# Kernel tuning notes

Hardware: AMD Instinct MI355X
Metric: run time of the kernel (lower is better)

## Reference

```python
import jax, jax.numpy as jnp
import numpy as np

N, H, C, G = 50000, 16, 8, 128   # nodes, heads, per-head channels, graphs
F_IN, NUM_CLASSES = 128, 2
E = 800000
HC = H * C
NEG_SLOPE = 0.2
BN_EPS = 1e-5


def setup_inputs() -> dict:
    key = jax.random.key(0)
    ks = jax.random.split(key, 32)
    s = 0.1
    p = lambda k, shape: (jax.random.normal(k, shape, jnp.float32) * s)
    inp = {
        "x": jax.random.normal(ks[0], (N, F_IN), jnp.float32),
        "edge_index": jax.random.randint(ks[1], (2, E), 0, N, dtype=jnp.int32),
        "batch": jnp.sort(jax.random.randint(ks[2], (N,), 0, G, dtype=jnp.int32)),
        # GAT layer 1 (in=F_IN)
        "W1": p(ks[3], (F_IN, HC)), "b1": p(ks[4], (HC,)),
        "asrc1": p(ks[5], (H, C)), "adst1": p(ks[6], (H, C)),
        "g1": 1.0 + p(ks[7], (HC,)), "beta1": p(ks[8], (HC,)),
        # GAT layer 2 (in=HC)
        "W2": p(ks[9], (HC, HC)), "b2": p(ks[10], (HC,)),
        "asrc2": p(ks[11], (H, C)), "adst2": p(ks[12], (H, C)),
        "g2": 1.0 + p(ks[13], (HC,)), "beta2": p(ks[14], (HC,)),
        # GAT layer 3
        "W3": p(ks[15], (HC, HC)), "b3": p(ks[16], (HC,)),
        "asrc3": p(ks[17], (H, C)), "adst3": p(ks[18], (H, C)),
        "g3": 1.0 + p(ks[19], (HC,)), "beta3": p(ks[20], (HC,)),
        # final linear + bn4
        "Wl": p(ks[21], (2 * HC, NUM_CLASSES)), "bl": p(ks[22], (NUM_CLASSES,)),
        "g4": 1.0 + p(ks[23], (NUM_CLASSES,)), "beta4": p(ks[24], (NUM_CLASSES,)),
    }
    return inp


def _gat(x, src, dst, W, b, asrc, adst):
    # x: [N, F_in] -> h: [N, H, C]
    h = (x @ W).reshape(N, H, C)
    a_s = jnp.einsum("nhc,hc->nh", h, asrc)  # [N,H]
    a_d = jnp.einsum("nhc,hc->nh", h, adst)
    e = jax.nn.leaky_relu(a_s[src] + a_d[dst], NEG_SLOPE)  # [E',H]
    # per-destination softmax (every node has a self loop -> segments non-empty)
    e_max = jax.ops.segment_max(e, dst, num_segments=N)
    ex = jnp.exp(e - e_max[dst])
    denom = jax.ops.segment_sum(ex, dst, num_segments=N)
    alpha = ex / (denom[dst] + 1e-16)  # [E',H]
    out = jax.ops.segment_sum(h[src] * alpha[:, :, None], dst, num_segments=N)
    return out.reshape(N, HC) + b


def _bn(x, g, beta):
    mu = jnp.mean(x, axis=0)
    var = jnp.mean((x - mu) ** 2, axis=0)  # biased, training-mode BN
    return (x - mu) * jax.lax.rsqrt(var + BN_EPS) * g + beta


def reference(x, edge_index, batch,
              W1, b1, asrc1, adst1, g1, beta1,
              W2, b2, asrc2, adst2, g2, beta2,
              W3, b3, asrc3, adst3, g3, beta3,
              Wl, bl, g4, beta4):
    # add self loops once (add_self_loops=True in every GATConv)
    loop = jnp.arange(N, dtype=edge_index.dtype)
    src = jnp.concatenate([edge_index[0], loop])
    dst = jnp.concatenate([edge_index[1], loop])

    h = jax.nn.relu(_bn(_gat(x, src, dst, W1, b1, asrc1, adst1), g1, beta1))
    h = jax.nn.relu(_bn(_gat(h, src, dst, W2, b2, asrc2, adst2), g2, beta2))
    h = jax.nn.relu(_bn(_gat(h, src, dst, W3, b3, asrc3, adst3), g3, beta3))

    pooled_sum = jax.ops.segment_sum(h, batch, num_segments=G)        # [G,HC]
    cnt = jax.ops.segment_sum(jnp.ones((N,), h.dtype), batch, num_segments=G)
    pooled_mean = pooled_sum / jnp.maximum(cnt, 1.0)[:, None]
    z = jnp.concatenate([pooled_mean, pooled_sum], axis=1)            # [G,2*HC]
    z = z @ Wl + bl
    return _bn(z, g4, beta4)
```

## Files before the change

kernel.cpp:

```cpp
#include <hip/hip_runtime.h>

#define NN 50000
#define NHEADS 16
#define NGRAPH 128
#define NEDGE 800000
#define NEP (NEDGE + NN)

#define EPB 2048
#define NBLK 416
#define NBUK 391
#define CASTB 3125
#define WTB 192
#define WASB 48

typedef float4 f4;
typedef __attribute__((ext_vector_type(4))) float f32x4;
typedef __attribute__((ext_vector_type(8))) short s8;

__device__ inline unsigned short f2b(float f) {
  union { float f; unsigned u; } v; v.f = f;
  unsigned r = v.u + 0x7FFFu + ((v.u >> 16) & 1u);
  return (unsigned short)(r >> 16);
}
__device__ inline float b2f(unsigned u16) {
  union { unsigned u; float f; } v; v.u = u16 << 16;
  return v.f;
}
__device__ inline float blo(unsigned u) {
  union { unsigned u; float f; } v; v.u = u << 16;
  return v.f;
}
__device__ inline float bhi(unsigned u) {
  union { unsigned u; float f; } v; v.u = u & 0xffff0000u;
  return v.f;
}


__global__ __launch_bounds__(256) void k_bhist(const int* __restrict__ ei, int* __restrict__ cntmat) {
  __shared__ int hist[NBUK];
  int t = threadIdx.x, b = blockIdx.x;
  for (int k = t; k < NBUK; k += 256) hist[k] = 0;
  __syncthreads();
  int i0 = b * EPB;
  int i1 = i0 + EPB < NEP ? i0 + EPB : NEP;
  for (int i = i0 + t; i < i1; i += 256) {
    int d = (i < NEDGE) ? ei[NEDGE + i] : (i - NEDGE);
    atomicAdd(&hist[d >> 7], 1);
  }
  __syncthreads();
  for (int k = t; k < NBUK; k += 256) cntmat[b * NBUK + k] = hist[k];
}

__global__ __launch_bounds__(512) void k_bscan(int* __restrict__ cntmat, int* __restrict__ btotal) {
  __shared__ int buf[512];
  int t = threadIdx.x, k = blockIdx.x;
  int v = (t < NBLK) ? cntmat[t * NBUK + k] : 0;
  buf[t] = v;
  __syncthreads();
  for (int off = 1; off < 512; off <<= 1) {
    int y = (t >= off) ? buf[t - off] : 0;
    __syncthreads();
    buf[t] += y;
    __syncthreads();
  }
  if (t < NBLK) cntmat[t * NBUK + k] = buf[t] - v;
  if (t == 511) btotal[k] = buf[511];
}

__global__ __launch_bounds__(512) void k_bbase(const int* __restrict__ btotal, int* __restrict__ bbase) {
  __shared__ int buf[512];
  int t = threadIdx.x;
  int v = (t < NBUK) ? btotal[t] : 0;
  buf[t] = v;
  __syncthreads();
  for (int off = 1; off < 512; off <<= 1) {
    int y = (t >= off) ? buf[t - off] : 0;
    __syncthreads();
    buf[t] += y;
    __syncthreads();
  }
  if (t < NBUK) bbase[t] = buf[t] - v;
  if (t == 511) bbase[NBUK] = buf[511];
}

__global__ __launch_bounds__(256) void k_bscatter(const int* __restrict__ ei, const int* __restrict__ cntmat,
                                                  const int* __restrict__ bbase, unsigned* __restrict__ pairs) {
  __shared__ int cur[NBUK];
  int t = threadIdx.x, b = blockIdx.x;
  for (int k = t; k < NBUK; k += 256) cur[k] = bbase[k] + cntmat[b * NBUK + k];
  __syncthreads();
  int i0 = b * EPB;
  int i1 = i0 + EPB < NEP ? i0 + EPB : NEP;
  for (int i = i0 + t; i < i1; i += 256) {
    int s, d;
    if (i < NEDGE) { s = ei[i]; d = ei[NEDGE + i]; }
    else { s = d = i - NEDGE; }
    int pos = atomicAdd(&cur[d >> 7], 1);
    pairs[pos] = ((unsigned)(d & 127) << 16) | (unsigned)s;
  }
}

__global__ __launch_bounds__(256) void k_bfinal(const unsigned* __restrict__ pairs, const int* __restrict__ bbase,
                                                int* __restrict__ row_off, int* __restrict__ colp) {
  __shared__ int cnt[128];
  __shared__ int buf[128];
  __shared__ int cur[128];
  int t = threadIdx.x, k = blockIdx.x;
  int n0 = k << 7;
  if (t < 128) cnt[t] = 0;
  __syncthreads();
  int p0 = bbase[k], p1 = bbase[k + 1];
  for (int i = p0 + t; i < p1; i += 256) atomicAdd(&cnt[pairs[i] >> 16], 1);
  __syncthreads();
  if (t < 128) buf[t] = cnt[t];
  __syncthreads();
  for (int off = 1; off < 128; off <<= 1) {
    int y = (t < 128 && t >= off) ? buf[t - off] : 0;
    __syncthreads();
    if (t < 128) buf[t] += y;
    __syncthreads();
  }
  if (t < 128) {
    int excl = buf[t] - cnt[t];
    cur[t] = p0 + excl;
    if (n0 + t < NN) row_off[n0 + t] = p0 + excl;
  }
  if (k == NBUK - 1 && t == 0) row_off[NN] = p1;
  __syncthreads();
  for (int i = p0 + t; i < p1; i += 256) {
    unsigned r = pairs[i];
    int pos = atomicAdd(&cur[r >> 16], 1);
    colp[pos] = (int)(r & 0xffffu);
  }
}


__global__ __launch_bounds__(256) void k_prep(const float* __restrict__ X, unsigned short* __restrict__ Xb,
                                              const float* __restrict__ W0, const float* __restrict__ W1, const float* __restrict__ W2,
                                              const float* __restrict__ as0, const float* __restrict__ as1, const float* __restrict__ as2,
                                              const float* __restrict__ ad0, const float* __restrict__ ad1, const float* __restrict__ ad2,
                                              unsigned short* __restrict__ T0, unsigned short* __restrict__ T1, unsigned short* __restrict__ T2,
                                              const int* __restrict__ batch, int* __restrict__ gstart) {
  int b = blockIdx.x, t = threadIdx.x;
  if (b < CASTB) {
    int i = b * 256 + t;
    const f4* X4 = (const f4*)X;
    f4 a = X4[2 * i], c = X4[2 * i + 1];
    uint4 o;
    o.x = (unsigned)f2b(a.x) | ((unsigned)f2b(a.y) << 16);
    o.y = (unsigned)f2b(a.z) | ((unsigned)f2b(a.w) << 16);
    o.z = (unsigned)f2b(c.x) | ((unsigned)f2b(c.y) << 16);
    o.w = (unsigned)f2b(c.z) | ((unsigned)f2b(c.w) << 16);
    ((uint4*)Xb)[i] = o;
  } else if (b < CASTB + WTB) {
    int idx = (b - CASTB) * 256 + t;
    int L = idx >> 14, r = idx & 16383;
    int n = r >> 7, kk = r & 127;
    const float* W = (L == 0) ? W0 : (L == 1) ? W1 : W2;
    unsigned short* T = (L == 0) ? T0 : (L == 1) ? T1 : T2;
    T[n * 128 + kk] = f2b(W[kk * 128 + n]);
  } else if (b < CASTB + WTB + WASB) {
    int idx = (b - CASTB - WTB) * 256 + t;
    int L = idx >> 12, r = idx & 4095;
    int h2 = r >> 7, kk = r & 127;
    int h = h2 & 15;
    const float* W = (L == 0) ? W0 : (L == 1) ? W1 : W2;
    const float* av = (h2 < 16) ? ((L == 0) ? as0 : (L == 1) ? as1 : as2)
                                : ((L == 0) ? ad0 : (L == 1) ? ad1 : ad2);
    unsigned short* T = (L == 0) ? T0 : (L == 1) ? T1 : T2;
    float s = 0.f;
#pragma unroll
    for (int c = 0; c < 8; ++c) s += W[kk * 128 + h * 8 + c] * av[h * 8 + c];
    T[(128 + h2) * 128 + kk] = f2b(s);
  } else {
    int g = t;
    if (g > NGRAPH) return;
    int lo = 0, hi = NN;
    while (lo < hi) { int mid = (lo + hi) >> 1; if (batch[mid] < g) lo = mid + 1; else hi = mid; }
    gstart[g] = lo;
  }
}


template<int FUSE>
__global__ __launch_bounds__(256) void k_gemm_t(const unsigned short* __restrict__ A, const unsigned short* __restrict__ Wt,
                                                const float* __restrict__ sc, unsigned short* __restrict__ Hb,
                                                unsigned short* __restrict__ Asb, float* __restrict__ Ad) {
  int w = threadIdx.x >> 6, l = threadIdx.x & 63;
  int r0 = blockIdx.x * 128 + w * 32;
  int lr = l & 15, lg = l >> 4;
  f32x4 acc[2][10];
#pragma unroll
  for (int m = 0; m < 2; ++m)
#pragma unroll
    for (int n = 0; n < 10; ++n) acc[m][n] = (f32x4){0.f, 0.f, 0.f, 0.f};

#pragma unroll
  for (int ks = 0; ks < 4; ++ks) {
    int koff = ks * 32 + lg * 8;
    s8 a[2];
    if constexpr (FUSE) {
      f4 s0 = *(const f4*)(sc + koff),       s1 = *(const f4*)(sc + koff + 4);
      f4 h0 = *(const f4*)(sc + 128 + koff), h1 = *(const f4*)(sc + 128 + koff + 4);
#pragma unroll
      for (int m = 0; m < 2; ++m) {
        int row = r0 + m * 16 + lr;
        row = (row < NN) ? row : (NN - 1);
        uint4 raw = *(const uint4*)(A + (size_t)row * 128 + koff);
        float v0 = fmaxf(blo(raw.x) * s0.x + h0.x, 0.f);
        float v1 = fmaxf(bhi(raw.x) * s0.y + h0.y, 0.f);
        float v2 = fmaxf(blo(raw.y) * s0.z + h0.z, 0.f);
        float v3 = fmaxf(bhi(raw.y) * s0.w + h0.w, 0.f);
        float v4 = fmaxf(blo(raw.z) * s1.x + h1.x, 0.f);
        float v5 = fmaxf(bhi(raw.z) * s1.y + h1.y, 0.f);
        float v6 = fmaxf(blo(raw.w) * s1.z + h1.z, 0.f);
        float v7 = fmaxf(bhi(raw.w) * s1.w + h1.w, 0.f);
        union { s8 v; uint4 u; } pk;
        pk.u.x = (unsigned)f2b(v0) | ((unsigned)f2b(v1) << 16);
        pk.u.y = (unsigned)f2b(v2) | ((unsigned)f2b(v3) << 16);
        pk.u.z = (unsigned)f2b(v4) | ((unsigned)f2b(v5) << 16);
        pk.u.w = (unsigned)f2b(v6) | ((unsigned)f2b(v7) << 16);
        a[m] = pk.v;
      }
    } else {
#pragma unroll
      for (int m = 0; m < 2; ++m) {
        int row = r0 + m * 16 + lr;
        row = (row < NN) ? row : (NN - 1);
        a[m] = *(const s8*)(A + (size_t)row * 128 + koff);
      }
    }
#pragma unroll
    for (int n = 0; n < 10; ++n) {
      s8 b = *(const s8*)(Wt + (size_t)(n * 16 + lr) * 128 + koff);
#pragma unroll
      for (int m = 0; m < 2; ++m)
        acc[m][n] = __builtin_amdgcn_mfma_f32_16x16x32_bf16(a[m], b, acc[m][n], 0, 0, 0);
    }
  }

#pragma unroll
  for (int m = 0; m < 2; ++m) {
    int rowb = r0 + m * 16 + lg * 4;
#pragma unroll
    for (int n = 0; n < 8; ++n) {
      int colb = n * 16 + lr;
#pragma unroll
      for (int reg = 0; reg < 4; ++reg) {
        int row = rowb + reg;
        if (row < NN) Hb[(size_t)row * 128 + colb] = f2b(acc[m][n][reg]);
      }
    }
#pragma unroll
    for (int reg = 0; reg < 4; ++reg) {
      int row = rowb + reg;
      if (row < NN) {
        Asb[row * 16 + lr] = f2b(acc[m][8][reg]);
        Ad[row * 16 + lr] = acc[m][9][reg];
      }
    }
  }
}


__global__ __launch_bounds__(256, 4) void k_agg(const unsigned short* __restrict__ Hb, const unsigned short* __restrict__ Asb,
                                                const float* __restrict__ Ad,
                                                const int* __restrict__ row_off, const int* __restrict__ col,
                                                unsigned short* __restrict__ Vb) {
  int node = blockIdx.x * 16 + (threadIdx.x >> 4);
  int h = threadIdx.x & 15;
  int e0 = row_off[node], e1 = row_off[node + 1];
  float adh = Ad[node * 16 + h];
  float den = 0.f;
  float acc[8] = {0.f, 0.f, 0.f, 0.f, 0.f, 0.f, 0.f, 0.f};
  int j = e0;
  for (; j + 7 < e1; j += 8) {
    int s[8];
#pragma unroll
    for (int q = 0; q < 8; ++q) s[q] = col[j + q];
    float a[8];
#pragma unroll
    for (int q = 0; q < 8; ++q) a[q] = b2f(Asb[s[q] * 16 + h]);
    uint4 p[8];
#pragma unroll
    for (int q = 0; q < 8; ++q) p[q] = *(const uint4*)(Hb + (size_t)s[q] * 128 + h * 8);
#pragma unroll
    for (int q = 0; q < 8; ++q) {
      float e = a[q] + adh;
      e = (e > 0.f) ? e : 0.2f * e;
      a[q] = __expf(e);
      den += a[q];
    }
#pragma unroll
    for (int q = 0; q < 8; ++q) {
      acc[0] += a[q] * blo(p[q].x); acc[1] += a[q] * bhi(p[q].x);
      acc[2] += a[q] * blo(p[q].y); acc[3] += a[q] * bhi(p[q].y);
      acc[4] += a[q] * blo(p[q].z); acc[5] += a[q] * bhi(p[q].z);
      acc[6] += a[q] * blo(p[q].w); acc[7] += a[q] * bhi(p[q].w);
    }
  }
  for (; j + 3 < e1; j += 4) {
    int s[4];
#pragma unroll
    for (int q = 0; q < 4; ++q) s[q] = col[j + q];
    float a[4];
#pragma unroll
    for (int q = 0; q < 4; ++q) a[q] = b2f(Asb[s[q] * 16 + h]);
    uint4 p[4];
#pragma unroll
    for (int q = 0; q < 4; ++q) p[q] = *(const uint4*)(Hb + (size_t)s[q] * 128 + h * 8);
#pragma unroll
    for (int q = 0; q < 4; ++q) {
      float e = a[q] + adh;
      e = (e > 0.f) ? e : 0.2f * e;
      a[q] = __expf(e);
      den += a[q];
    }
#pragma unroll
    for (int q = 0; q < 4; ++q) {
      acc[0] += a[q] * blo(p[q].x); acc[1] += a[q] * bhi(p[q].x);
      acc[2] += a[q] * blo(p[q].y); acc[3] += a[q] * bhi(p[q].y);
      acc[4] += a[q] * blo(p[q].z); acc[5] += a[q] * bhi(p[q].z);
      acc[6] += a[q] * blo(p[q].w); acc[7] += a[q] * bhi(p[q].w);
    }
  }
  for (; j < e1; ++j) {
    int s0 = col[j];
    float a0 = b2f(Asb[s0 * 16 + h]) + adh;
    uint4 p0 = *(const uint4*)(Hb + (size_t)s0 * 128 + h * 8);
    a0 = (a0 > 0.f) ? a0 : 0.2f * a0;
    float x0 = __expf(a0);
    den += x0;
    acc[0] += x0 * blo(p0.x); acc[1] += x0 * bhi(p0.x);
    acc[2] += x0 * blo(p0.y); acc[3] += x0 * bhi(p0.y);
    acc[4] += x0 * blo(p0.z); acc[5] += x0 * bhi(p0.z);
    acc[6] += x0 * blo(p0.w); acc[7] += x0 * bhi(p0.w);
  }
  float inv = 1.f / (den + 1e-16f);
  uint4 o;
  o.x = (unsigned)f2b(acc[0] * inv) | ((unsigned)f2b(acc[1] * inv) << 16);
  o.y = (unsigned)f2b(acc[2] * inv) | ((unsigned)f2b(acc[3] * inv) << 16);
  o.z = (unsigned)f2b(acc[4] * inv) | ((unsigned)f2b(acc[5] * inv) << 16);
  o.w = (unsigned)f2b(acc[6] * inv) | ((unsigned)f2b(acc[7] * inv) << 16);
  *(uint4*)(Vb + (size_t)node * 128 + h * 8) = o;
}


#define BN_CHUNK 391

__global__ __launch_bounds__(256) void k_bnreduce(const unsigned short* __restrict__ Vb, float* __restrict__ partS, float* __restrict__ partQ) {
  int t = threadIdx.x;
  int c4 = t & 31, rs = t >> 5;
  int r0 = blockIdx.x * BN_CHUNK + rs;
  int rend = blockIdx.x * BN_CHUNK + BN_CHUNK;
  if (rend > NN) rend = NN;
  float s0 = 0.f, s1 = 0.f, s2 = 0.f, s3 = 0.f;
  float q0 = 0.f, q1 = 0.f, q2 = 0.f, q3 = 0.f;
  for (int r = r0; r < rend; r += 8) {
    uint2 p = *(const uint2*)(Vb + (size_t)r * 128 + c4 * 4);
    float v0 = blo(p.x), v1 = bhi(p.x);
    float v2 = blo(p.y), v3 = bhi(p.y);
    s0 += v0; s1 += v1; s2 += v2; s3 += v3;
    q0 += v0 * v0; q1 += v1 * v1; q2 += v2 * v2; q3 += v3 * v3;
  }
  __shared__ float sm[8][32][8];
  sm[rs][c4][0] = s0; sm[rs][c4][1] = s1; sm[rs][c4][2] = s2; sm[rs][c4][3] = s3;
  sm[rs][c4][4] = q0; sm[rs][c4][5] = q1; sm[rs][c4][6] = q2; sm[rs][c4][7] = q3;
  __syncthreads();
  if (t < 32) {
#pragma unroll
    for (int k = 0; k < 4; ++k) {
      float S = 0.f, Q = 0.f;
#pragma unroll
      for (int r = 0; r < 8; ++r) { S += sm[r][t][k]; Q += sm[r][t][4 + k]; }
      partS[blockIdx.x * 128 + t * 4 + k] = S;
      partQ[blockIdx.x * 128 + t * 4 + k] = Q;
    }
  }
}

__global__ __launch_bounds__(512) void k_bnfin(const float* __restrict__ partS, const float* __restrict__ partQ,
                                               const float* __restrict__ gam, const float* __restrict__ bet,
                                               float* __restrict__ sc) {
  int t = threadIdx.x;
  int c = t & 127, q = (t >> 7) & 1, hf = t >> 8;
  const float* src = q ? partQ : partS;
  float s = 0.f;
#pragma unroll 8
  for (int i = hf * 64; i < hf * 64 + 64; ++i) s += src[i * 128 + c];
  __shared__ float sm[512];
  sm[t] = s;
  __syncthreads();
  if (t < 128) {
    float S = sm[t] + sm[t + 256];
    float Q = sm[t + 128] + sm[t + 384];
    float mean = S * (1.f / NN);
    float var = fmaxf(Q * (1.f / NN) - mean * mean, 0.f);
    float sg = gam[t] * rsqrtf(var + 1e-5f);
    sc[t] = sg;
    sc[128 + t] = bet[t] - mean * sg;
  }
}


__global__ __launch_bounds__(256) void k_pool(const unsigned short* __restrict__ Vb, const float* __restrict__ sc,
                                              const int* __restrict__ gstart, float* __restrict__ pp) {
  int g = blockIdx.x >> 2, chunk = blockIdx.x & 3;
  int t = threadIdx.x;
  int c4 = t & 31, rs = t >> 5;
  f4 s = ((const f4*)sc)[c4], sh = ((const f4*)sc)[32 + c4];
  int r0 = gstart[g], r1 = gstart[g + 1];
  float s0 = 0.f, s1 = 0.f, s2 = 0.f, s3 = 0.f;
  for (int r = r0 + chunk + 4 * rs; r < r1; r += 32) {
    uint2 p = *(const uint2*)(Vb + (size_t)r * 128 + c4 * 4);
    s0 += fmaxf(blo(p.x) * s.x + sh.x, 0.f);
    s1 += fmaxf(bhi(p.x) * s.y + sh.y, 0.f);
    s2 += fmaxf(blo(p.y) * s.z + sh.z, 0.f);
    s3 += fmaxf(bhi(p.y) * s.w + sh.w, 0.f);
  }
  __shared__ float sm[8][32][4];
  sm[rs][c4][0] = s0; sm[rs][c4][1] = s1; sm[rs][c4][2] = s2; sm[rs][c4][3] = s3;
  __syncthreads();
  if (t < 32) {
#pragma unroll
    for (int k = 0; k < 4; ++k) {
      float S = 0.f;
#pragma unroll
      for (int r = 0; r < 8; ++r) S += sm[r][t][k];
      pp[(size_t)blockIdx.x * 128 + t * 4 + k] = S;
    }
  }
}

__global__ __launch_bounds__(256) void k_final(const float* __restrict__ pp, const int* __restrict__ gstart,
                                               const float* __restrict__ Wl, const float* __restrict__ bl,
                                               const float* __restrict__ g4, const float* __restrict__ b4,
                                               float* __restrict__ out) {
  int t = threadIdx.x;
  int g = t >> 1, cls = t & 1;
  float cnt = fmaxf((float)(gstart[g + 1] - gstart[g]), 1.f);
  float inv = 1.f / cnt;
  float z = bl[cls];
  for (int f = 0; f < 128; ++f) {
    float ps = pp[(size_t)(g * 4 + 0) * 128 + f] + pp[(size_t)(g * 4 + 1) * 128 + f]
             + pp[(size_t)(g * 4 + 2) * 128 + f] + pp[(size_t)(g * 4 + 3) * 128 + f];
    z += ps * inv * Wl[f * 2 + cls] + ps * Wl[(128 + f) * 2 + cls];
  }
  __shared__ float zs[256];
  __shared__ float st[4];
  zs[t] = z;
  __syncthreads();
  if (t < 2) {
    float s = 0.f, s2 = 0.f;
    for (int gg = 0; gg < 128; ++gg) { float v = zs[gg * 2 + t]; s += v; s2 += v * v; }
    float mean = s * (1.f / 128.f);
    float var = s2 * (1.f / 128.f) - mean * mean;
    var = fmaxf(var, 0.f);
    float sc = g4[t] * rsqrtf(var + 1e-5f);
    st[t] = sc; st[2 + t] = b4[t] - mean * sc;
  }
  __syncthreads();
  out[t] = zs[t] * st[cls] + st[2 + cls];
}


extern "C" void kernel_launch(void* const* d_in, const int* in_sizes, int n_in,
                              void* d_out, int out_size, void* d_ws, size_t ws_size,
                              hipStream_t stream) {
  const float* x     = (const float*)d_in[0];
  const int*   ei    = (const int*)d_in[1];
  const int*   batch = (const int*)d_in[2];
  const float* W[3]    = {(const float*)d_in[3],  (const float*)d_in[9],  (const float*)d_in[15]};
  const float* asrc[3] = {(const float*)d_in[5],  (const float*)d_in[11], (const float*)d_in[17]};
  const float* adst[3] = {(const float*)d_in[6],  (const float*)d_in[12], (const float*)d_in[18]};
  const float* gam[3]  = {(const float*)d_in[7],  (const float*)d_in[13], (const float*)d_in[19]};
  const float* bet[3]  = {(const float*)d_in[8],  (const float*)d_in[14], (const float*)d_in[20]};
  const float* Wl    = (const float*)d_in[21];
  const float* bl    = (const float*)d_in[22];
  const float* g4    = (const float*)d_in[23];
  const float* beta4 = (const float*)d_in[24];

  char* ws = (char*)d_ws;
  size_t off = 0;
  auto alloc = [&](size_t bytes) -> void* {
    void* p = (void*)(ws + off);
    off += (bytes + 255) & ~(size_t)255;
    return p;
  };

  int* row_off  = (int*)alloc((size_t)(NN + 1) * 4);
  int* col      = (int*)alloc((size_t)NEP * 4);
  int* cntmat   = (int*)alloc((size_t)NBLK * NBUK * 4);
  int* btotal   = (int*)alloc((size_t)NBUK * 4);
  int* bbase    = (int*)alloc((size_t)(NBUK + 1) * 4);
  unsigned* pairs = (unsigned*)alloc((size_t)NEP * 4);
  unsigned short* Xb = (unsigned short*)alloc((size_t)NN * 128 * 2);
  unsigned short* Hb = (unsigned short*)alloc((size_t)NN * 128 * 2);
  unsigned short* Vb = (unsigned short*)alloc((size_t)NN * 128 * 2);
  unsigned short* Asb = (unsigned short*)alloc((size_t)NN * 16 * 2);
  float* Ad     = (float*)alloc((size_t)NN * 16 * 4);
  unsigned short* Wt0 = (unsigned short*)alloc((size_t)160 * 128 * 2);
  unsigned short* Wt1 = (unsigned short*)alloc((size_t)160 * 128 * 2);
  unsigned short* Wt2 = (unsigned short*)alloc((size_t)160 * 128 * 2);
  const unsigned short* Wt[3] = {Wt0, Wt1, Wt2};
  float* partS  = (float*)alloc(128 * 128 * 4);
  float* partQ  = (float*)alloc(128 * 128 * 4);
  float* bn_sc  = (float*)alloc(256 * 4);
  float* pp     = (float*)alloc((size_t)NGRAPH * 4 * 128 * 4);
  int* gstart   = (int*)alloc((size_t)(NGRAPH + 1) * 4);

  k_bhist<<<NBLK, 256, 0, stream>>>(ei, cntmat);
  k_bscan<<<NBUK, 512, 0, stream>>>(cntmat, btotal);
  k_bbase<<<1, 512, 0, stream>>>(btotal, bbase);
  k_bscatter<<<NBLK, 256, 0, stream>>>(ei, cntmat, bbase, pairs);
  k_bfinal<<<NBUK, 256, 0, stream>>>(pairs, bbase, row_off, col);

  k_prep<<<CASTB + WTB + WASB + 1, 256, 0, stream>>>(x, Xb, W[0], W[1], W[2],
                                                     asrc[0], asrc[1], asrc[2], adst[0], adst[1], adst[2],
                                                     Wt0, Wt1, Wt2, batch, gstart);

  for (int L = 0; L < 3; ++L) {
    if (L == 0)
      k_gemm_t<0><<<(NN + 127) / 128, 256, 0, stream>>>(Xb, Wt[L], nullptr, Hb, Asb, Ad);
    else
      k_gemm_t<1><<<(NN + 127) / 128, 256, 0, stream>>>(Vb, Wt[L], bn_sc, Hb, Asb, Ad);
    k_agg<<<NN / 16, 256, 0, stream>>>(Hb, Asb, Ad, row_off, col, Vb);
    k_bnreduce<<<128, 256, 0, stream>>>(Vb, partS, partQ);
    k_bnfin<<<1, 512, 0, stream>>>(partS, partQ, gam[L], bet[L], bn_sc);
  }

  k_pool<<<NGRAPH * 4, 256, 0, stream>>>(Vb, bn_sc, gstart, pp);
  k_final<<<1, 256, 0, stream>>>(pp, gstart, Wl, bl, g4, beta4, (float*)d_out);
}
```

Measured before the change: 297.4 us.

## Split GAT aggregation edges across two half-warps with double-buffered loads

The aggregation kernel now gives each destination node 32 lanes: two groups of 16 heads each take alternating edges, and their partial sums and denominators are combined with a lane shuffle. The main loop is software-pipelined with two register buffers, so the gathers for the next 4 edges are issued before the current 4 are consumed. The aim is more memory-level parallelism and less serial latency per node, since average degree is about 17. The costs are twice as many threads and blocks, extra shuffles, half the lanes idle during the store, and higher register pressure from the double buffers.

New measurement: 301.9 us. About the same (+1.5%).

```diff
diff --git a/kernel.cpp b/kernel.cpp
--- a/kernel.cpp
+++ b/kernel.cpp
@@ -263,68 +263,57 @@
 }
 
 
+#define AGG_LOAD(S, A, P) do { \
+  _Pragma("unroll") for (int q = 0; q < 4; ++q) S[q] = col[j + 2 * q]; \
+  _Pragma("unroll") for (int q = 0; q < 4; ++q) A[q] = b2f(Asb[S[q] * 16 + h]); \
+  _Pragma("unroll") for (int q = 0; q < 4; ++q) P[q] = *(const uint4*)(Hb + (size_t)S[q] * 128 + h * 8); \
+  j += 8; } while (0)
+
+#define AGG_CONSUME(A, P) do { \
+  _Pragma("unroll") for (int q = 0; q < 4; ++q) { \
+    float e = A[q] + adh; e = (e > 0.f) ? e : 0.2f * e; A[q] = __expf(e); den += A[q]; } \
+  _Pragma("unroll") for (int q = 0; q < 4; ++q) { \
+    acc[0] += A[q] * blo(P[q].x); acc[1] += A[q] * bhi(P[q].x); \
+    acc[2] += A[q] * blo(P[q].y); acc[3] += A[q] * bhi(P[q].y); \
+    acc[4] += A[q] * blo(P[q].z); acc[5] += A[q] * bhi(P[q].z); \
+    acc[6] += A[q] * blo(P[q].w); acc[7] += A[q] * bhi(P[q].w); } } while (0)
+
 __global__ __launch_bounds__(256, 4) void k_agg(const unsigned short* __restrict__ Hb, const unsigned short* __restrict__ Asb,
                                                 const float* __restrict__ Ad,
                                                 const int* __restrict__ row_off, const int* __restrict__ col,
                                                 unsigned short* __restrict__ Vb) {
-  int node = blockIdx.x * 16 + (threadIdx.x >> 4);
-  int h = threadIdx.x & 15;
+  int node = blockIdx.x * 8 + (threadIdx.x >> 5);
+  int l = threadIdx.x & 31;
+  int h = l & 15, par = l >> 4;
   int e0 = row_off[node], e1 = row_off[node + 1];
   float adh = Ad[node * 16 + h];
   float den = 0.f;
   float acc[8] = {0.f, 0.f, 0.f, 0.f, 0.f, 0.f, 0.f, 0.f};
-  int j = e0;
-  for (; j + 7 < e1; j += 8) {
-    int s[8];
-#pragma unroll
-    for (int q = 0; q < 8; ++q) s[q] = col[j + q];
-    float a[8];
-#pragma unroll
-    for (int q = 0; q < 8; ++q) a[q] = b2f(Asb[s[q] * 16 + h]);
-    uint4 p[8];
-#pragma unroll
-    for (int q = 0; q < 8; ++q) p[q] = *(const uint4*)(Hb + (size_t)s[q] * 128 + h * 8);
-#pragma unroll
-    for (int q = 0; q < 8; ++q) {
-      float e = a[q] + adh;
-      e = (e > 0.f) ? e : 0.2f * e;
-      a[q] = __expf(e);
-      den += a[q];
-    }
-#pragma unroll
-    for (int q = 0; q < 8; ++q) {
-      acc[0] += a[q] * blo(p[q].x); acc[1] += a[q] * bhi(p[q].x);
-      acc[2] += a[q] * blo(p[q].y); acc[3] += a[q] * bhi(p[q].y);
-      acc[4] += a[q] * blo(p[q].z); acc[5] += a[q] * bhi(p[q].z);
-      acc[6] += a[q] * blo(p[q].w); acc[7] += a[q] * bhi(p[q].w);
-    }
-  }
-  for (; j + 3 < e1; j += 4) {
-    int s[4];
-#pragma unroll
-    for (int q = 0; q < 4; ++q) s[q] = col[j + q];
-    float a[4];
-#pragma unroll
-    for (int q = 0; q < 4; ++q) a[q] = b2f(Asb[s[q] * 16 + h]);
-    uint4 p[4];
-#pragma unroll
-    for (int q = 0; q < 4; ++q) p[q] = *(const uint4*)(Hb + (size_t)s[q] * 128 + h * 8);
-#pragma unroll
-    for (int q = 0; q < 4; ++q) {
-      float e = a[q] + adh;
-      e = (e > 0.f) ? e : 0.2f * e;
-      a[q] = __expf(e);
-      den += a[q];
-    }
-#pragma unroll
-    for (int q = 0; q < 4; ++q) {
-      acc[0] += a[q] * blo(p[q].x); acc[1] += a[q] * bhi(p[q].x);
-      acc[2] += a[q] * blo(p[q].y); acc[3] += a[q] * bhi(p[q].y);
-      acc[4] += a[q] * blo(p[q].z); acc[5] += a[q] * bhi(p[q].z);
-      acc[6] += a[q] * blo(p[q].w); acc[7] += a[q] * bhi(p[q].w);
-    }
-  }
-  for (; j < e1; ++j) {
+  int j = e0 + par;
+
+  int sA[4]; float aA[4]; uint4 pA[4];
+  int sB[4]; float aB[4]; uint4 pB[4];
+  (void)sA; (void)sB;
+  if (j + 6 < e1) {
+    AGG_LOAD(sA, aA, pA);
+    for (;;) {
+      if (j + 6 < e1) {
+        AGG_LOAD(sB, aB, pB);
+        AGG_CONSUME(aA, pA);
+      } else {
+        AGG_CONSUME(aA, pA);
+        break;
+      }
+      if (j + 6 < e1) {
+        AGG_LOAD(sA, aA, pA);
+        AGG_CONSUME(aB, pB);
+      } else {
+        AGG_CONSUME(aB, pB);
+        break;
+      }
+    }
+  }
+  for (; j < e1; j += 2) {
     int s0 = col[j];
     float a0 = b2f(Asb[s0 * 16 + h]) + adh;
     uint4 p0 = *(const uint4*)(Hb + (size_t)s0 * 128 + h * 8);
@@ -336,13 +325,18 @@
     acc[4] += x0 * blo(p0.z); acc[5] += x0 * bhi(p0.z);
     acc[6] += x0 * blo(p0.w); acc[7] += x0 * bhi(p0.w);
   }
-  float inv = 1.f / (den + 1e-16f);
-  uint4 o;
-  o.x = (unsigned)f2b(acc[0] * inv) | ((unsigned)f2b(acc[1] * inv) << 16);
-  o.y = (unsigned)f2b(acc[2] * inv) | ((unsigned)f2b(acc[3] * inv) << 16);
-  o.z = (unsigned)f2b(acc[4] * inv) | ((unsigned)f2b(acc[5] * inv) << 16);
-  o.w = (unsigned)f2b(acc[6] * inv) | ((unsigned)f2b(acc[7] * inv) << 16);
-  *(uint4*)(Vb + (size_t)node * 128 + h * 8) = o;
+  den += __shfl_xor(den, 16);
+#pragma unroll
+  for (int k = 0; k < 8; ++k) acc[k] += __shfl_xor(acc[k], 16);
+  if (par == 0) {
+    float inv = 1.f / (den + 1e-16f);
+    uint4 o;
+    o.x = (unsigned)f2b(acc[0] * inv) | ((unsigned)f2b(acc[1] * inv) << 16);
+    o.y = (unsigned)f2b(acc[2] * inv) | ((unsigned)f2b(acc[3] * inv) << 16);
+    o.z = (unsigned)f2b(acc[4] * inv) | ((unsigned)f2b(acc[5] * inv) << 16);
+    o.w = (unsigned)f2b(acc[6] * inv) | ((unsigned)f2b(acc[7] * inv) << 16);
+    *(uint4*)(Vb + (size_t)node * 128 + h * 8) = o;
+  }
 }
 
 
@@ -524,7 +518,7 @@
       k_gemm_t<0><<<(NN + 127) / 128, 256, 0, stream>>>(Xb, Wt[L], nullptr, Hb, Asb, Ad);
     else
       k_gemm_t<1><<<(NN + 127) / 128, 256, 0, stream>>>(Vb, Wt[L], bn_sc, Hb, Asb, Ad);
-    k_agg<<<NN / 16, 256, 0, stream>>>(Hb, Asb, Ad, row_off, col, Vb);
+    k_agg<<<NN / 8, 256, 0, stream>>>(Hb, Asb, Ad, row_off, col, Vb);
     k_bnreduce<<<128, 256, 0, stream>>>(Vb, partS, partQ);
     k_bnfin<<<1, 512, 0, stream>>>(partS, partQ, gam[L], bet[L], bn_sc);
   }
```

## Split GAT aggregation by head halves and edge parity; merge histogram with prep kernel

Applied to the files above, without the earlier changes.

The edge-histogram kernel and the input/weight prep kernel are merged into one launch, removing a launch and letting independent work share the GPU. The aggregation kernel now covers each node with two blocks, one per half of the heads. Within a block, two lanes per head take alternating edges, and their partial sums are combined with a cross-lane shuffle. This doubles the number of threads in flight to hide gather latency on high-degree nodes, at the cost of redundant row_off/Ad loads, a shuffle reduction, and a block-index mapping chosen so paired blocks stay adjacent for cache locality.

After: 282.2 us (median of 2 runs). 1.05x faster.

```diff
diff --git a/kernel.cpp b/kernel.cpp
--- a/kernel.cpp
+++ b/kernel.cpp
@@ -36,20 +36,68 @@
 }
 
 
-__global__ __launch_bounds__(256) void k_bhist(const int* __restrict__ ei, int* __restrict__ cntmat) {
+__global__ __launch_bounds__(256) void k_front(const int* __restrict__ ei, int* __restrict__ cntmat,
+                                               const float* __restrict__ X, unsigned short* __restrict__ Xb,
+                                               const float* __restrict__ W0, const float* __restrict__ W1, const float* __restrict__ W2,
+                                               const float* __restrict__ as0, const float* __restrict__ as1, const float* __restrict__ as2,
+                                               const float* __restrict__ ad0, const float* __restrict__ ad1, const float* __restrict__ ad2,
+                                               unsigned short* __restrict__ T0, unsigned short* __restrict__ T1, unsigned short* __restrict__ T2,
+                                               const int* __restrict__ batch, int* __restrict__ gstart) {
   __shared__ int hist[NBUK];
-  int t = threadIdx.x, b = blockIdx.x;
-  for (int k = t; k < NBUK; k += 256) hist[k] = 0;
-  __syncthreads();
-  int i0 = b * EPB;
-  int i1 = i0 + EPB < NEP ? i0 + EPB : NEP;
-  for (int i = i0 + t; i < i1; i += 256) {
-    int d = (i < NEDGE) ? ei[NEDGE + i] : (i - NEDGE);
-    atomicAdd(&hist[d >> 7], 1);
-  }
-  __syncthreads();
-  for (int k = t; k < NBUK; k += 256) cntmat[b * NBUK + k] = hist[k];
-}
+  int b = blockIdx.x, t = threadIdx.x;
+  if (b < NBLK) {
+    for (int k = t; k < NBUK; k += 256) hist[k] = 0;
+    __syncthreads();
+    int i0 = b * EPB;
+    int i1 = i0 + EPB < NEP ? i0 + EPB : NEP;
+    for (int i = i0 + t; i < i1; i += 256) {
+      int d = (i < NEDGE) ? ei[NEDGE + i] : (i - NEDGE);
+      atomicAdd(&hist[d >> 7], 1);
+    }
+    __syncthreads();
+    for (int k = t; k < NBUK; k += 256) cntmat[b * NBUK + k] = hist[k];
+    return;
+  }
+  int pb = b - NBLK;
+  if (pb < CASTB) {
+    int i = pb * 256 + t;
+    const f4* X4 = (const f4*)X;
+    f4 a = X4[2 * i], c = X4[2 * i + 1];
+    uint4 o;
+    o.x = (unsigned)f2b(a.x) | ((unsigned)f2b(a.y) << 16);
+    o.y = (unsigned)f2b(a.z) | ((unsigned)f2b(a.w) << 16);
+    o.z = (unsigned)f2b(c.x) | ((unsigned)f2b(c.y) << 16);
+    o.w = (unsigned)f2b(c.z) | ((unsigned)f2b(c.w) << 16);
+    ((uint4*)Xb)[i] = o;
+  } else if (pb < CASTB + WTB) {
+    int idx = (pb - CASTB) * 256 + t;
+    int L = idx >> 14, r = idx & 16383;
+    int n = r >> 7, kk = r & 127;
+    const float* W = (L == 0) ? W0 : (L == 1) ? W1 : W2;
+    unsigned short* T = (L == 0) ? T0 : (L == 1) ? T1 : T2;
+    T[n * 128 + kk] = f2b(W[kk * 128 + n]);
+  } else if (pb < CASTB + WTB + WASB) {
+    int idx = (pb - CASTB - WTB) * 256 + t;
+    int L = idx >> 12, r = idx & 4095;
+    int h2 = r >> 7, kk = r & 127;
+    int h = h2 & 15;
+    const float* W = (L == 0) ? W0 : (L == 1) ? W1 : W2;
+    const float* av = (h2 < 16) ? ((L == 0) ? as0 : (L == 1) ? as1 : as2)
+                                : ((L == 0) ? ad0 : (L == 1) ? ad1 : ad2);
+    unsigned short* T = (L == 0) ? T0 : (L == 1) ? T1 : T2;
+    float s = 0.f;
+#pragma unroll
+    for (int c = 0; c < 8; ++c) s += W[kk * 128 + h * 8 + c] * av[h * 8 + c];
+    T[(128 + h2) * 128 + kk] = f2b(s);
+  } else {
+    int g = t;
+    if (g > NGRAPH) return;
+    int lo = 0, hi = NN;
+    while (lo < hi) { int mid = (lo + hi) >> 1; if (batch[mid] < g) lo = mid + 1; else hi = mid; }
+    gstart[g] = lo;
+  }
+}
+
 
 __global__ __launch_bounds__(512) void k_bscan(int* __restrict__ cntmat, int* __restrict__ btotal) {
   __shared__ int buf[512];
@@ -131,53 +179,6 @@
     unsigned r = pairs[i];
     int pos = atomicAdd(&cur[r >> 16], 1);
     colp[pos] = (int)(r & 0xffffu);
-  }
-}
-
-
-__global__ __launch_bounds__(256) void k_prep(const float* __restrict__ X, unsigned short* __restrict__ Xb,
-                                              const float* __restrict__ W0, const float* __restrict__ W1, const float* __restrict__ W2,
-                                              const float* __restrict__ as0, const float* __restrict__ as1, const float* __restrict__ as2,
-                                              const float* __restrict__ ad0, const float* __restrict__ ad1, const float* __restrict__ ad2,
-                                              unsigned short* __restrict__ T0, unsigned short* __restrict__ T1, unsigned short* __restrict__ T2,
-                                              const int* __restrict__ batch, int* __restrict__ gstart) {
-  int b = blockIdx.x, t = threadIdx.x;
-  if (b < CASTB) {
-    int i = b * 256 + t;
-    const f4* X4 = (const f4*)X;
-    f4 a = X4[2 * i], c = X4[2 * i + 1];
-    uint4 o;
-    o.x = (unsigned)f2b(a.x) | ((unsigned)f2b(a.y) << 16);
-    o.y = (unsigned)f2b(a.z) | ((unsigned)f2b(a.w) << 16);
-    o.z = (unsigned)f2b(c.x) | ((unsigned)f2b(c.y) << 16);
-    o.w = (unsigned)f2b(c.z) | ((unsigned)f2b(c.w) << 16);
-    ((uint4*)Xb)[i] = o;
-  } else if (b < CASTB + WTB) {
-    int idx = (b - CASTB) * 256 + t;
-    int L = idx >> 14, r = idx & 16383;
-    int n = r >> 7, kk = r & 127;
-    const float* W = (L == 0) ? W0 : (L == 1) ? W1 : W2;
-    unsigned short* T = (L == 0) ? T0 : (L == 1) ? T1 : T2;
-    T[n * 128 + kk] = f2b(W[kk * 128 + n]);
-  } else if (b < CASTB + WTB + WASB) {
-    int idx = (b - CASTB - WTB) * 256 + t;
-    int L = idx >> 12, r = idx & 4095;
-    int h2 = r >> 7, kk = r & 127;
-    int h = h2 & 15;
-    const float* W = (L == 0) ? W0 : (L == 1) ? W1 : W2;
-    const float* av = (h2 < 16) ? ((L == 0) ? as0 : (L == 1) ? as1 : as2)
-                                : ((L == 0) ? ad0 : (L == 1) ? ad1 : ad2);
-    unsigned short* T = (L == 0) ? T0 : (L == 1) ? T1 : T2;
-    float s = 0.f;
-#pragma unroll
-    for (int c = 0; c < 8; ++c) s += W[kk * 128 + h * 8 + c] * av[h * 8 + c];
-    T[(128 + h2) * 128 + kk] = f2b(s);
-  } else {
-    int g = t;
-    if (g > NGRAPH) return;
-    int lo = 0, hi = NN;
-    while (lo < hi) { int mid = (lo + hi) >> 1; if (batch[mid] < g) lo = mid + 1; else hi = mid; }
-    gstart[g] = lo;
   }
 }
 
@@ -267,17 +268,24 @@
                                                 const float* __restrict__ Ad,
                                                 const int* __restrict__ row_off, const int* __restrict__ col,
                                                 unsigned short* __restrict__ Vb) {
-  int node = blockIdx.x * 16 + (threadIdx.x >> 4);
-  int h = threadIdx.x & 15;
+  int b = blockIdx.x;
+  int half = (b >> 2) & 1;
+  int nb = (b >> 3) * 4 + (b & 3);
+  if (nb >= 3125) return;
+  int t = threadIdx.x;
+  int node = nb * 16 + (t >> 4);
+  int l = t & 15;
+  int h = half * 8 + (l & 7);
+  int par = l >> 3;
   int e0 = row_off[node], e1 = row_off[node + 1];
   float adh = Ad[node * 16 + h];
   float den = 0.f;
   float acc[8] = {0.f, 0.f, 0.f, 0.f, 0.f, 0.f, 0.f, 0.f};
-  int j = e0;
-  for (; j + 7 < e1; j += 8) {
+  int j = e0 + par;
+  for (; j + 14 < e1; j += 16) {
     int s[8];
 #pragma unroll
-    for (int q = 0; q < 8; ++q) s[q] = col[j + q];
+    for (int q = 0; q < 8; ++q) s[q] = col[j + 2 * q];
     float a[8];
 #pragma unroll
     for (int q = 0; q < 8; ++q) a[q] = b2f(Asb[s[q] * 16 + h]);
@@ -299,10 +307,10 @@
       acc[6] += a[q] * blo(p[q].w); acc[7] += a[q] * bhi(p[q].w);
     }
   }
-  for (; j + 3 < e1; j += 4) {
+  for (; j + 6 < e1; j += 8) {
     int s[4];
 #pragma unroll
-    for (int q = 0; q < 4; ++q) s[q] = col[j + q];
+    for (int q = 0; q < 4; ++q) s[q] = col[j + 2 * q];
     float a[4];
 #pragma unroll
     for (int q = 0; q < 4; ++q) a[q] = b2f(Asb[s[q] * 16 + h]);
@@ -324,7 +332,7 @@
       acc[6] += a[q] * blo(p[q].w); acc[7] += a[q] * bhi(p[q].w);
     }
   }
-  for (; j < e1; ++j) {
+  for (; j < e1; j += 2) {
     int s0 = col[j];
     float a0 = b2f(Asb[s0 * 16 + h]) + adh;
     uint4 p0 = *(const uint4*)(Hb + (size_t)s0 * 128 + h * 8);
@@ -336,13 +344,18 @@
     acc[4] += x0 * blo(p0.z); acc[5] += x0 * bhi(p0.z);
     acc[6] += x0 * blo(p0.w); acc[7] += x0 * bhi(p0.w);
   }
-  float inv = 1.f / (den + 1e-16f);
-  uint4 o;
-  o.x = (unsigned)f2b(acc[0] * inv) | ((unsigned)f2b(acc[1] * inv) << 16);
-  o.y = (unsigned)f2b(acc[2] * inv) | ((unsigned)f2b(acc[3] * inv) << 16);
-  o.z = (unsigned)f2b(acc[4] * inv) | ((unsigned)f2b(acc[5] * inv) << 16);
-  o.w = (unsigned)f2b(acc[6] * inv) | ((unsigned)f2b(acc[7] * inv) << 16);
-  *(uint4*)(Vb + (size_t)node * 128 + h * 8) = o;
+  den += __shfl_xor(den, 8);
+#pragma unroll
+  for (int k = 0; k < 8; ++k) acc[k] += __shfl_xor(acc[k], 8);
+  if (par == 0) {
+    float inv = 1.f / (den + 1e-16f);
+    uint4 o;
+    o.x = (unsigned)f2b(acc[0] * inv) | ((unsigned)f2b(acc[1] * inv) << 16);
+    o.y = (unsigned)f2b(acc[2] * inv) | ((unsigned)f2b(acc[3] * inv) << 16);
+    o.z = (unsigned)f2b(acc[4] * inv) | ((unsigned)f2b(acc[5] * inv) << 16);
+    o.w = (unsigned)f2b(acc[6] * inv) | ((unsigned)f2b(acc[7] * inv) << 16);
+    *(uint4*)(Vb + (size_t)node * 128 + h * 8) = o;
+  }
 }
 
 
@@ -509,22 +522,20 @@
   float* pp     = (float*)alloc((size_t)NGRAPH * 4 * 128 * 4);
   int* gstart   = (int*)alloc((size_t)(NGRAPH + 1) * 4);
 
-  k_bhist<<<NBLK, 256, 0, stream>>>(ei, cntmat);
+  k_front<<<NBLK + CASTB + WTB + WASB + 1, 256, 0, stream>>>(ei, cntmat, x, Xb, W[0], W[1], W[2],
+                                                             asrc[0], asrc[1], asrc[2], adst[0], adst[1], adst[2],
+                                                             Wt0, Wt1, Wt2, batch, gstart);
   k_bscan<<<NBUK, 512, 0, stream>>>(cntmat, btotal);
   k_bbase<<<1, 512, 0, stream>>>(btotal, bbase);
   k_bscatter<<<NBLK, 256, 0, stream>>>(ei, cntmat, bbase, pairs);
   k_bfinal<<<NBUK, 256, 0, stream>>>(pairs, bbase, row_off, col);
-
-  k_prep<<<CASTB + WTB + WASB + 1, 256, 0, stream>>>(x, Xb, W[0], W[1], W[2],
-                                                     asrc[0], asrc[1], asrc[2], adst[0], adst[1], adst[2],
-                                                     Wt0, Wt1, Wt2, batch, gstart);
 
   for (int L = 0; L < 3; ++L) {
     if (L == 0)
       k_gemm_t<0><<<(NN + 127) / 128, 256, 0, stream>>>(Xb, Wt[L], nullptr, Hb, Asb, Ad);
     else
       k_gemm_t<1><<<(NN + 127) / 128, 256, 0, stream>>>(Vb, Wt[L], bn_sc, Hb, Asb, Ad);
-    k_agg<<<NN / 16, 256, 0, stream>>>(Hb, Asb, Ad, row_off, col, Vb);
+    k_agg<<<6256, 256, 0, stream>>>(Hb, Asb, Ad, row_off, col, Vb);
     k_bnreduce<<<128, 256, 0, stream>>>(Vb, partS, partQ);
     k_bnfin<<<1, 512, 0, stream>>>(partS, partQ, gam[L], bet[L], bn_sc);
   }
```
